# Kernel optimization log

Hardware: AMD Instinct MI355X
Metric: run time of the kernel (lower is better)

## Reference

```python
import jax, jax.numpy as jnp
import numpy as np

AGENT, WIN, DIM, HEADS = 6, 7, 256, 8


def _relative_position_index():
    # Exactly mirrors the torch buffer construction (meshgrid indexing='ij').
    coords = np.stack(np.meshgrid(np.arange(AGENT), np.arange(WIN), np.arange(WIN), indexing='ij'))
    cf = coords.reshape(3, -1)  # (3, N)
    rel = cf[:, :, None] - cf[:, None, :]  # (3, N, N)
    rel = np.transpose(rel, (1, 2, 0)).copy()  # (N, N, 3)
    rel[..., 0] += AGENT - 1
    rel[..., 1] += WIN - 1
    rel[..., 2] += WIN - 1
    rel[..., 0] *= (2 * WIN - 1) * (2 * WIN - 1)
    rel[..., 1] *= 2 * WIN - 1
    return rel.sum(-1).astype(np.int32)  # (N, N)


def setup_inputs() -> dict:
    key = jax.random.key(0)
    k1, k2, k3, k4 = jax.random.split(key, 4)
    b, X, Y = 1, 16, 16
    table_size = (2 * AGENT - 1) * (2 * WIN - 1) * (2 * WIN - 1)  # 1859
    x = jax.random.normal(k1, (b, AGENT, X, Y, WIN, WIN, DIM), dtype=jnp.float32)
    w_qkv = jax.random.normal(k2, (DIM, 3 * DIM), dtype=jnp.float32) * 0.02
    w_out = jax.random.normal(k3, (DIM, DIM), dtype=jnp.float32) * 0.02
    bias_table = jax.random.normal(k4, (table_size, HEADS), dtype=jnp.float32) * 0.02
    rel_index = jnp.asarray(_relative_position_index())
    return {"x": x, "w_qkv": w_qkv, "w_out": w_out, "bias_table": bias_table, "rel_index": rel_index}


def reference(x, w_qkv, w_out, bias_table, rel_index):
    b, L, X, Y, W1, W2, D = x.shape
    h = bias_table.shape[-1]
    dh = D // h
    scale = dh ** -0.5
    N = L * W1 * W2
    B = b * X * Y
    # 'b l x y w1 w2 d -> (b x y) (l w1 w2) d'
    xw = jnp.transpose(x, (0, 2, 3, 1, 4, 5, 6)).reshape(B, N, D)
    qkv = xw @ w_qkv  # (B, N, 3D)
    q, k, v = jnp.split(qkv, 3, axis=-1)
    def heads(t):
        return jnp.transpose(t.reshape(B, N, h, dh), (0, 2, 1, 3))  # (B, h, N, dh)
    q, k, v = heads(q) * scale, heads(k), heads(v)
    sim = jnp.einsum('bhid,bhjd->bhij', q, k)  # (B, h, N, N)
    bias = bias_table[rel_index]  # (N, N, h)
    sim = sim + jnp.transpose(bias, (2, 0, 1))[None]
    attn = jax.nn.softmax(sim, axis=-1)
    out = jnp.einsum('bhij,bhjd->bhid', attn, v)  # (B, h, N, dh)
    out = jnp.transpose(out, (0, 2, 1, 3)).reshape(B, N, h * dh)
    out = out @ w_out  # (B, N, D)
    out = out.reshape(b, X, Y, L, W1, W2, D)
    return jnp.transpose(out, (0, 3, 1, 2, 4, 5, 6))  # (b, l, x, y, w1, w2, d)
```

## Files before the change

kernel.cpp:

```cpp
#include <hip/hip_runtime.h>
#include <hip/hip_bf16.h>

#define NTOK 294
#define NB   256
#define NN   (NTOK*NTOK)
#define ROWS_M (NB*NTOK)
#define USN  19267584ULL

typedef __bf16 bf16x8 __attribute__((ext_vector_type(8)));
typedef float  f32x4  __attribute__((ext_vector_type(4)));
typedef unsigned short ushort_t;

union Bf8 { bf16x8 v; unsigned short u[8]; };

__device__ inline unsigned short f2bf(float f) {
    unsigned int u = __float_as_uint(f);
    return (unsigned short)((u + 0x7FFFu + ((u >> 16) & 1u)) >> 16);
}

__global__ void bias_expand(const float* __restrict__ table,
                            const int* __restrict__ rel,
                            float* __restrict__ biasQ) {
    int t = blockIdx.x * 256 + threadIdx.x;
    if (t >= NN) return;
    int idx = rel[t];
    const float* src = table + idx * 8;
#pragma unroll
    for (int h = 0; h < 8; ++h)
        biasQ[h * NN + t] = src[h];
}

__global__ __launch_bounds__(256) void qkv_gemm_mfma(const float* __restrict__ x,
                                                     const float* __restrict__ wqkv,
                                                     ushort_t* __restrict__ qb,
                                                     ushort_t* __restrict__ kb,
                                                     ushort_t* __restrict__ vt) {
    __shared__ unsigned short As[128 * 64];
    __shared__ unsigned short Bs[128 * 64];
    const int t    = threadIdx.x;
    const int lane = t & 63;
    const int w    = t >> 6;
    const int wm   = w >> 1, wn = w & 1;

    const int r  = t >> 1;
    const int h2 = t & 1;
    int m  = blockIdx.x * 128 + r;
    int Bi = m / NTOK, n = m - Bi * NTOK;
    int l  = n / 49,   ww = n - l * 49;
    int xx = Bi >> 4,  yy = Bi & 15;
    const float* arow = x + (size_t)((((l * 16 + xx) * 16 + yy) * 49 + ww) << 8) + h2 * 32;

    const int n4  = (t & 31) * 4;
    const int kl0 = (t >> 5) * 8;
    const int cb  = blockIdx.y * 128;
    const float* bsrc = wqkv + (size_t)kl0 * 768 + cb + n4;

    f32x4 acc[4][4];
#pragma unroll
    for (int i = 0; i < 4; ++i)
#pragma unroll
        for (int j = 0; j < 4; ++j) acc[i][j] = (f32x4){0.f, 0.f, 0.f, 0.f};

    for (int kk = 0; kk < 256; kk += 64) {
        Bf8 apk[4];
#pragma unroll
        for (int c = 0; c < 4; ++c) {
            float4 f0 = *(const float4*)(arow + kk + c * 8);
            float4 f1 = *(const float4*)(arow + kk + c * 8 + 4);
            apk[c].u[0] = f2bf(f0.x); apk[c].u[1] = f2bf(f0.y);
            apk[c].u[2] = f2bf(f0.z); apk[c].u[3] = f2bf(f0.w);
            apk[c].u[4] = f2bf(f1.x); apk[c].u[5] = f2bf(f1.y);
            apk[c].u[6] = f2bf(f1.z); apk[c].u[7] = f2bf(f1.w);
        }
        float bv[8][4];
#pragma unroll
        for (int e = 0; e < 8; ++e) {
            float4 f = *(const float4*)(bsrc + (size_t)(kk + e) * 768);
            bv[e][0] = f.x; bv[e][1] = f.y; bv[e][2] = f.z; bv[e][3] = f.w;
        }
        __syncthreads();
#pragma unroll
        for (int c = 0; c < 4; ++c) {
            int idx = (r * 64 + h2 * 32 + c * 8) ^ ((r & 7) << 3);
            *(bf16x8*)&As[idx] = apk[c].v;
        }
#pragma unroll
        for (int j = 0; j < 4; ++j) {
            Bf8 pk;
#pragma unroll
            for (int e = 0; e < 8; ++e) pk.u[e] = f2bf(bv[e][j]);
            int nn  = n4 + j;
            int idx = (nn * 64 + kl0) ^ ((nn & 7) << 3);
            *(bf16x8*)&Bs[idx] = pk.v;
        }
        __syncthreads();
        const int lrow = lane & 15;
        const int kofs = (lane >> 4) * 8;
#pragma unroll
        for (int ks = 0; ks < 2; ++ks) {
            bf16x8 af[4], bfr[4];
#pragma unroll
            for (int fi = 0; fi < 4; ++fi) {
                int rr  = wm * 64 + fi * 16 + lrow;
                int idx = (rr * 64 + ks * 32 + kofs) ^ ((rr & 7) << 3);
                af[fi] = *(const bf16x8*)&As[idx];
            }
#pragma unroll
            for (int fj = 0; fj < 4; ++fj) {
                int rr  = wn * 64 + fj * 16 + lrow;
                int idx = (rr * 64 + ks * 32 + kofs) ^ ((rr & 7) << 3);
                bfr[fj] = *(const bf16x8*)&Bs[idx];
            }
#pragma unroll
            for (int fi = 0; fi < 4; ++fi)
#pragma unroll
                for (int fj = 0; fj < 4; ++fj)
                    acc[fi][fj] = __builtin_amdgcn_mfma_f32_16x16x32_bf16(
                        af[fi], bfr[fj], acc[fi][fj], 0, 0, 0);
        }
    }

    const float scale = 0.17677669529663687f;
    const int rq   = lane >> 4;
    const int cidx = lane & 15;
#pragma unroll
    for (int fi = 0; fi < 4; ++fi) {
#pragma unroll
        for (int reg = 0; reg < 4; ++reg) {
            int mm  = blockIdx.x * 128 + wm * 64 + fi * 16 + rq * 4 + reg;
            int Bi2 = mm / NTOK, n2 = mm - Bi2 * NTOK;
#pragma unroll
            for (int fj = 0; fj < 4; ++fj) {
                int c     = cb + wn * 64 + fj * 16 + cidx;
                int which = c >> 8;
                int rr    = c & 255;
                int hh    = rr >> 5, di = rr & 31;
                int bhi   = Bi2 * 8 + hh;
                if (which == 0) {
                    qb[((size_t)bhi * NTOK + n2) * 32 + di] = f2bf(acc[fi][fj][reg] * scale);
                } else if (which == 1) {
                    kb[((size_t)bhi * NTOK + n2) * 32 + di] = f2bf(acc[fi][fj][reg]);
                } else {
                    vt[((size_t)bhi * 32 + di) * NTOK + n2] = f2bf(acc[fi][fj][reg]);
                }
            }
        }
    }
}

#define S_KS 40
#define S_VS 328
#define S_PS 40
__global__ __launch_bounds__(256) void attn_mfma(ushort_t* __restrict__ qb,
                                                 const ushort_t* __restrict__ kb,
                                                 const ushort_t* __restrict__ vt,
                                                 const float* __restrict__ biasQ) {
    __shared__ ushort_t ks[320 * S_KS];
    __shared__ ushort_t vs[32 * S_VS];
    __shared__ ushort_t ps[4 * 16 * S_PS];
    const int qt = blockIdx.x, bh = blockIdx.y, h = bh & 7;
    const int tid = threadIdx.x;

    const unsigned int* ksrc = (const unsigned int*)(kb + (size_t)bh * NTOK * 32);
    for (int t = tid; t < 294 * 16; t += 256) {
        int r = t >> 4, i = t & 15;
        *(unsigned int*)&ks[r * S_KS + 2 * i] = ksrc[t];
    }
    for (int t = tid; t < 26 * 16; t += 256) {
        int r = 294 + (t >> 4), i = t & 15;
        *(unsigned int*)&ks[r * S_KS + 2 * i] = 0u;
    }
    const unsigned int* vsrc = (const unsigned int*)(vt + (size_t)bh * 32 * NTOK);
    for (int t = tid; t < 32 * 147; t += 256) {
        int d = t / 147, i = t - d * 147;
        *(unsigned int*)&vs[d * S_VS + 2 * i] = vsrc[t];
    }
    for (int t = tid; t < 32 * 17; t += 256) {
        int d = t / 17, i = 147 + (t - d * 17);
        *(unsigned int*)&vs[d * S_VS + 2 * i] = 0u;
    }
    __syncthreads();

    const int wave = tid >> 6, lane = tid & 63;
    const int c = lane & 15, g = lane >> 4;
    const int q0 = qt * 128 + wave * 32;

    bf16x8 qf[2];
#pragma unroll
    for (int qs = 0; qs < 2; ++qs) {
        int qa = q0 + qs * 16 + c; if (qa > 293) qa = 293;
        qf[qs] = *(const bf16x8*)&qb[((size_t)bh * NTOK + qa) * 32 + 8 * g];
    }
    f32x4 acc_o[2][2];
    float psum[2][4];
#pragma unroll
    for (int qs = 0; qs < 2; ++qs) {
#pragma unroll
        for (int hf = 0; hf < 2; ++hf) acc_o[qs][hf] = (f32x4){0.f, 0.f, 0.f, 0.f};
#pragma unroll
        for (int rg = 0; rg < 4; ++rg) psum[qs][rg] = 0.f;
    }
    ushort_t* pw = ps + wave * 16 * S_PS;
    const float* bbase = biasQ + (size_t)h * NN;

    for (int kt = 0; kt < 10; ++kt) {
        const int kbase = kt * 32;
        bf16x8 kf[2], vf[2];
#pragma unroll
        for (int ksub = 0; ksub < 2; ++ksub)
            kf[ksub] = *(const bf16x8*)&ks[(kbase + ksub * 16 + c) * S_KS + 8 * g];
#pragma unroll
        for (int hf = 0; hf < 2; ++hf)
            vf[hf] = *(const bf16x8*)&vs[(hf * 16 + c) * S_VS + kbase + 8 * g];

#pragma unroll
        for (int qs = 0; qs < 2; ++qs) {
            f32x4 s0 = __builtin_amdgcn_mfma_f32_16x16x32_bf16(
                qf[qs], kf[0], (f32x4){0.f, 0.f, 0.f, 0.f}, 0, 0, 0);
            f32x4 s1 = __builtin_amdgcn_mfma_f32_16x16x32_bf16(
                qf[qs], kf[1], (f32x4){0.f, 0.f, 0.f, 0.f}, 0, 0, 0);
            const int qrb = q0 + qs * 16 + g * 4;
#pragma unroll
            for (int rg = 0; rg < 4; ++rg) {
                int qa = qrb + rg; if (qa > 293) qa = 293;
                const float* bp = bbase + (size_t)qa * NTOK;
#pragma unroll
                for (int ksub = 0; ksub < 2; ++ksub) {
                    int ka = kbase + ksub * 16 + c;
                    int kc = ka > 293 ? 293 : ka;
                    float bias = (ka < NTOK) ? bp[kc] : -1e4f;
                    float s = (ksub ? s1[rg] : s0[rg]) + bias;
                    float p = __expf(s);
                    psum[qs][rg] += p;
                    pw[(g * 4 + rg) * S_PS + ksub * 16 + c] = f2bf(p);
                }
            }
            bf16x8 pa = *(const bf16x8*)&pw[c * S_PS + 8 * g];
#pragma unroll
            for (int hf = 0; hf < 2; ++hf)
                acc_o[qs][hf] = __builtin_amdgcn_mfma_f32_16x16x32_bf16(
                    pa, vf[hf], acc_o[qs][hf], 0, 0, 0);
        }
    }

#pragma unroll
    for (int qs = 0; qs < 2; ++qs)
#pragma unroll
        for (int rg = 0; rg < 4; ++rg) {
            float v = psum[qs][rg];
            v += __shfl_xor(v, 1); v += __shfl_xor(v, 2);
            v += __shfl_xor(v, 4); v += __shfl_xor(v, 8);
            psum[qs][rg] = 1.0f / v;
        }

#pragma unroll
    for (int qs = 0; qs < 2; ++qs) {
        const int qrb = q0 + qs * 16 + g * 4;
#pragma unroll
        for (int rg = 0; rg < 4; ++rg) {
            int qa = qrb + rg;
            if (qa < NTOK) {
#pragma unroll
                for (int hf = 0; hf < 2; ++hf) {
                    float val = acc_o[qs][hf][rg] * psum[qs][rg];
                    qb[((size_t)bh * NTOK + qa) * 32 + hf * 16 + c] = f2bf(val);
                }
            }
        }
    }
}

__global__ __launch_bounds__(256) void out_gemm_mfma(const ushort_t* __restrict__ ob,
                                                     const float* __restrict__ wout,
                                                     float* __restrict__ out) {
    __shared__ unsigned short As[128 * 64];
    __shared__ unsigned short Bs[128 * 64];
    const int t    = threadIdx.x;
    const int lane = t & 63;
    const int w    = t >> 6;
    const int wm   = w >> 1, wn = w & 1;

    const int r  = t >> 1;
    const int h2 = t & 1;
    int m  = blockIdx.x * 128 + r;
    int Bi = m / NTOK, n = m - Bi * NTOK;

    const int n4  = (t & 31) * 4;
    const int kl0 = (t >> 5) * 8;
    const int cb  = blockIdx.y * 128;
    const float* bsrc = wout + (size_t)kl0 * 256 + cb + n4;

    f32x4 acc[4][4];
#pragma unroll
    for (int i = 0; i < 4; ++i)
#pragma unroll
        for (int j = 0; j < 4; ++j) acc[i][j] = (f32x4){0.f, 0.f, 0.f, 0.f};

    for (int kk = 0; kk < 256; kk += 64) {
        const int h_idx = (kk >> 5) + h2;
        const ushort_t* asrc = ob + ((size_t)(Bi * 8 + h_idx) * NTOK + n) * 32;
        bf16x8 apk[4];
#pragma unroll
        for (int c = 0; c < 4; ++c) apk[c] = *(const bf16x8*)&asrc[c * 8];
        float bv[8][4];
#pragma unroll
        for (int e = 0; e < 8; ++e) {
            float4 f = *(const float4*)(bsrc + (size_t)(kk + e) * 256);
            bv[e][0] = f.x; bv[e][1] = f.y; bv[e][2] = f.z; bv[e][3] = f.w;
        }
        __syncthreads();
#pragma unroll
        for (int c = 0; c < 4; ++c) {
            int idx = (r * 64 + h2 * 32 + c * 8) ^ ((r & 7) << 3);
            *(bf16x8*)&As[idx] = apk[c];
        }
#pragma unroll
        for (int j = 0; j < 4; ++j) {
            Bf8 pk;
#pragma unroll
            for (int e = 0; e < 8; ++e) pk.u[e] = f2bf(bv[e][j]);
            int nn  = n4 + j;
            int idx = (nn * 64 + kl0) ^ ((nn & 7) << 3);
            *(bf16x8*)&Bs[idx] = pk.v;
        }
        __syncthreads();
        const int lrow = lane & 15;
        const int kofs = (lane >> 4) * 8;
#pragma unroll
        for (int ks = 0; ks < 2; ++ks) {
            bf16x8 af[4], bfr[4];
#pragma unroll
            for (int fi = 0; fi < 4; ++fi) {
                int rr  = wm * 64 + fi * 16 + lrow;
                int idx = (rr * 64 + ks * 32 + kofs) ^ ((rr & 7) << 3);
                af[fi] = *(const bf16x8*)&As[idx];
            }
#pragma unroll
            for (int fj = 0; fj < 4; ++fj) {
                int rr  = wn * 64 + fj * 16 + lrow;
                int idx = (rr * 64 + ks * 32 + kofs) ^ ((rr & 7) << 3);
                bfr[fj] = *(const bf16x8*)&Bs[idx];
            }
#pragma unroll
            for (int fi = 0; fi < 4; ++fi)
#pragma unroll
                for (int fj = 0; fj < 4; ++fj)
                    acc[fi][fj] = __builtin_amdgcn_mfma_f32_16x16x32_bf16(
                        af[fi], bfr[fj], acc[fi][fj], 0, 0, 0);
        }
    }

    const int rq   = lane >> 4;
    const int cidx = lane & 15;
#pragma unroll
    for (int fi = 0; fi < 4; ++fi) {
#pragma unroll
        for (int reg = 0; reg < 4; ++reg) {
            int mm  = blockIdx.x * 128 + wm * 64 + fi * 16 + rq * 4 + reg;
            int Bi2 = mm / NTOK, n2 = mm - Bi2 * NTOK;
            int l2  = n2 / 49,   w2 = n2 - l2 * 49;
            int xx2 = Bi2 >> 4,  yy2 = Bi2 & 15;
            float* orow = out + (size_t)((((l2 * 16 + xx2) * 16 + yy2) * 49 + w2) << 8);
#pragma unroll
            for (int fj = 0; fj < 4; ++fj) {
                int c = cb + wn * 64 + fj * 16 + cidx;
                orow[c] = acc[fi][fj][reg];
            }
        }
    }
}

extern "C" void kernel_launch(void* const* d_in, const int* in_sizes, int n_in,
                              void* d_out, int out_size, void* d_ws, size_t ws_size,
                              hipStream_t stream) {
    const float* x     = (const float*)d_in[0];
    const float* wqkv  = (const float*)d_in[1];
    const float* wout  = (const float*)d_in[2];
    const float* table = (const float*)d_in[3];
    const int*   rel   = (const int*)d_in[4];
    float* out = (float*)d_out;

    ushort_t* qb    = (ushort_t*)d_ws;
    ushort_t* kb    = qb + USN;
    ushort_t* vt    = kb + USN;
    float*    biasQ = (float*)(vt + USN);

    hipLaunchKernelGGL(bias_expand, dim3((NN + 255) / 256), dim3(256), 0, stream,
                       table, rel, biasQ);
    hipLaunchKernelGGL(qkv_gemm_mfma, dim3(ROWS_M / 128, 6), dim3(256), 0, stream,
                       x, wqkv, qb, kb, vt);
    hipLaunchKernelGGL(attn_mfma, dim3(3, 2048), dim3(256), 0, stream,
                       qb, kb, vt, biasQ);
    hipLaunchKernelGGL(out_gemm_mfma, dim3(ROWS_M / 128, 2), dim3(256), 0, stream,
                       qb, wout, out);
}
```

Baseline: 430.4 us.

## Pre-transpose weights to bf16 and load MFMA fragments directly from global memory

Adds a prep kernel that converts and transposes w_qkv and w_out to bf16 once per call. The QKV and output GEMMs drop their shared-memory staging and barriers, and each lane loads its MFMA fragments straight from global memory. The grid is reordered so the column tiles of the same row block run adjacently and can share the cached A rows. This removes the LDS round-trip, the per-block weight conversion and the syncthreads, in exchange for redundant global/L2 traffic across waves and an extra small kernel launch.

```diff
diff --git a/kernel.cpp b/kernel.cpp
--- a/kernel.cpp
+++ b/kernel.cpp
@@ -16,6 +16,13 @@
 __device__ inline unsigned short f2bf(float f) {
     unsigned int u = __float_as_uint(f);
     return (unsigned short)((u + 0x7FFFu + ((u >> 16) & 1u)) >> 16);
+}
+
+__device__ inline bf16x8 cvt8(float4 a, float4 b) {
+    bf16x8 r;
+    r[0] = (__bf16)a.x; r[1] = (__bf16)a.y; r[2] = (__bf16)a.z; r[3] = (__bf16)a.w;
+    r[4] = (__bf16)b.x; r[5] = (__bf16)b.y; r[6] = (__bf16)b.z; r[7] = (__bf16)b.w;
+    return r;
 }
 
 __global__ void bias_expand(const float* __restrict__ table,
@@ -30,30 +37,49 @@
         biasQ[h * NN + t] = src[h];
 }
 
-__global__ __launch_bounds__(256) void qkv_gemm_mfma(const float* __restrict__ x,
-                                                     const float* __restrict__ wqkv,
-                                                     ushort_t* __restrict__ qb,
-                                                     ushort_t* __restrict__ kb,
-                                                     ushort_t* __restrict__ vt) {
-    __shared__ unsigned short As[128 * 64];
-    __shared__ unsigned short Bs[128 * 64];
+__global__ void wt_prep(const float* __restrict__ wqkv,
+                        const float* __restrict__ wout,
+                        ushort_t* __restrict__ wqkvT,
+                        ushort_t* __restrict__ woutT) {
+    int t = blockIdx.x * 256 + threadIdx.x;
+    if (t < 768 * 256) {
+        int n = t >> 8, k = t & 255;
+        wqkvT[t] = f2bf(wqkv[k * 768 + n]);
+    } else {
+        int u = t - 768 * 256;
+        int n = u >> 8, k = u & 255;
+        woutT[u] = f2bf(wout[k * 256 + n]);
+    }
+}
+
+__global__ __launch_bounds__(256) void qkv_gemm_mfma2(const float* __restrict__ x,
+                                                      const ushort_t* __restrict__ wqkvT,
+                                                      ushort_t* __restrict__ qb,
+                                                      ushort_t* __restrict__ kb,
+                                                      ushort_t* __restrict__ vt) {
     const int t    = threadIdx.x;
     const int lane = t & 63;
     const int w    = t >> 6;
     const int wm   = w >> 1, wn = w & 1;
-
-    const int r  = t >> 1;
-    const int h2 = t & 1;
-    int m  = blockIdx.x * 128 + r;
-    int Bi = m / NTOK, n = m - Bi * NTOK;
-    int l  = n / 49,   ww = n - l * 49;
-    int xx = Bi >> 4,  yy = Bi & 15;
-    const float* arow = x + (size_t)((((l * 16 + xx) * 16 + yy) * 49 + ww) << 8) + h2 * 32;
-
-    const int n4  = (t & 31) * 4;
-    const int kl0 = (t >> 5) * 8;
-    const int cb  = blockIdx.y * 128;
-    const float* bsrc = wqkv + (size_t)kl0 * 768 + cb + n4;
+    const int l15  = lane & 15, kg8 = (lane >> 4) * 8;
+    const int cb   = blockIdx.x * 128;
+    const int mt   = blockIdx.y * 128;
+
+    const float* arow[4];
+#pragma unroll
+    for (int fi = 0; fi < 4; ++fi) {
+        int m  = mt + wm * 64 + fi * 16 + l15;
+        int Bi = m / NTOK, n = m - Bi * NTOK;
+        int l  = n / 49,   ww = n - l * 49;
+        int xx = Bi >> 4,  yy = Bi & 15;
+        arow[fi] = x + (size_t)((((l * 16 + xx) * 16 + yy) * 49 + ww) << 8) + kg8;
+    }
+    const ushort_t* brow[4];
+#pragma unroll
+    for (int fj = 0; fj < 4; ++fj) {
+        int nn = cb + wn * 64 + fj * 16 + l15;
+        brow[fj] = wqkvT + (size_t)nn * 256 + kg8;
+    }
 
     f32x4 acc[4][4];
 #pragma unroll
@@ -61,63 +87,24 @@
 #pragma unroll
         for (int j = 0; j < 4; ++j) acc[i][j] = (f32x4){0.f, 0.f, 0.f, 0.f};
 
-    for (int kk = 0; kk < 256; kk += 64) {
-        Bf8 apk[4];
-#pragma unroll
-        for (int c = 0; c < 4; ++c) {
-            float4 f0 = *(const float4*)(arow + kk + c * 8);
-            float4 f1 = *(const float4*)(arow + kk + c * 8 + 4);
-            apk[c].u[0] = f2bf(f0.x); apk[c].u[1] = f2bf(f0.y);
-            apk[c].u[2] = f2bf(f0.z); apk[c].u[3] = f2bf(f0.w);
-            apk[c].u[4] = f2bf(f1.x); apk[c].u[5] = f2bf(f1.y);
-            apk[c].u[6] = f2bf(f1.z); apk[c].u[7] = f2bf(f1.w);
-        }
-        float bv[8][4];
-#pragma unroll
-        for (int e = 0; e < 8; ++e) {
-            float4 f = *(const float4*)(bsrc + (size_t)(kk + e) * 768);
-            bv[e][0] = f.x; bv[e][1] = f.y; bv[e][2] = f.z; bv[e][3] = f.w;
-        }
-        __syncthreads();
-#pragma unroll
-        for (int c = 0; c < 4; ++c) {
-            int idx = (r * 64 + h2 * 32 + c * 8) ^ ((r & 7) << 3);
-            *(bf16x8*)&As[idx] = apk[c].v;
-        }
-#pragma unroll
-        for (int j = 0; j < 4; ++j) {
-            Bf8 pk;
-#pragma unroll
-            for (int e = 0; e < 8; ++e) pk.u[e] = f2bf(bv[e][j]);
-            int nn  = n4 + j;
-            int idx = (nn * 64 + kl0) ^ ((nn & 7) << 3);
-            *(bf16x8*)&Bs[idx] = pk.v;
-        }
-        __syncthreads();
-        const int lrow = lane & 15;
-        const int kofs = (lane >> 4) * 8;
-#pragma unroll
-        for (int ks = 0; ks < 2; ++ks) {
-            bf16x8 af[4], bfr[4];
-#pragma unroll
-            for (int fi = 0; fi < 4; ++fi) {
-                int rr  = wm * 64 + fi * 16 + lrow;
-                int idx = (rr * 64 + ks * 32 + kofs) ^ ((rr & 7) << 3);
-                af[fi] = *(const bf16x8*)&As[idx];
-            }
-#pragma unroll
-            for (int fj = 0; fj < 4; ++fj) {
-                int rr  = wn * 64 + fj * 16 + lrow;
-                int idx = (rr * 64 + ks * 32 + kofs) ^ ((rr & 7) << 3);
-                bfr[fj] = *(const bf16x8*)&Bs[idx];
-            }
-#pragma unroll
-            for (int fi = 0; fi < 4; ++fi)
-#pragma unroll
-                for (int fj = 0; fj < 4; ++fj)
-                    acc[fi][fj] = __builtin_amdgcn_mfma_f32_16x16x32_bf16(
-                        af[fi], bfr[fj], acc[fi][fj], 0, 0, 0);
-        }
+#pragma unroll 2
+    for (int kk = 0; kk < 256; kk += 32) {
+        bf16x8 af[4], bfr[4];
+#pragma unroll
+        for (int fi = 0; fi < 4; ++fi) {
+            float4 f0 = *(const float4*)(arow[fi] + kk);
+            float4 f1 = *(const float4*)(arow[fi] + kk + 4);
+            af[fi] = cvt8(f0, f1);
+        }
+#pragma unroll
+        for (int fj = 0; fj < 4; ++fj)
+            bfr[fj] = *(const bf16x8*)(brow[fj] + kk);
+#pragma unroll
+        for (int fi = 0; fi < 4; ++fi)
+#pragma unroll
+            for (int fj = 0; fj < 4; ++fj)
+                acc[fi][fj] = __builtin_amdgcn_mfma_f32_16x16x32_bf16(
+                    af[fi], bfr[fj], acc[fi][fj], 0, 0, 0);
     }
 
     const float scale = 0.17677669529663687f;
@@ -127,7 +114,7 @@
     for (int fi = 0; fi < 4; ++fi) {
 #pragma unroll
         for (int reg = 0; reg < 4; ++reg) {
-            int mm  = blockIdx.x * 128 + wm * 64 + fi * 16 + rq * 4 + reg;
+            int mm  = mt + wm * 64 + fi * 16 + rq * 4 + reg;
             int Bi2 = mm / NTOK, n2 = mm - Bi2 * NTOK;
 #pragma unroll
             for (int fj = 0; fj < 4; ++fj) {
@@ -270,25 +257,30 @@
     }
 }
 
-__global__ __launch_bounds__(256) void out_gemm_mfma(const ushort_t* __restrict__ ob,
-                                                     const float* __restrict__ wout,
-                                                     float* __restrict__ out) {
-    __shared__ unsigned short As[128 * 64];
-    __shared__ unsigned short Bs[128 * 64];
+__global__ __launch_bounds__(256) void out_gemm_mfma2(const ushort_t* __restrict__ ob,
+                                                      const ushort_t* __restrict__ woutT,
+                                                      float* __restrict__ out) {
     const int t    = threadIdx.x;
     const int lane = t & 63;
     const int w    = t >> 6;
     const int wm   = w >> 1, wn = w & 1;
-
-    const int r  = t >> 1;
-    const int h2 = t & 1;
-    int m  = blockIdx.x * 128 + r;
-    int Bi = m / NTOK, n = m - Bi * NTOK;
-
-    const int n4  = (t & 31) * 4;
-    const int kl0 = (t >> 5) * 8;
-    const int cb  = blockIdx.y * 128;
-    const float* bsrc = wout + (size_t)kl0 * 256 + cb + n4;
+    const int l15  = lane & 15, kg8 = (lane >> 4) * 8;
+    const int cb   = blockIdx.x * 128;
+    const int mt   = blockIdx.y * 128;
+
+    const ushort_t* abase[4];
+#pragma unroll
+    for (int fi = 0; fi < 4; ++fi) {
+        int m  = mt + wm * 64 + fi * 16 + l15;
+        int Bi = m / NTOK, n = m - Bi * NTOK;
+        abase[fi] = ob + ((size_t)(Bi * 8) * NTOK + n) * 32 + kg8;
+    }
+    const ushort_t* brow[4];
+#pragma unroll
+    for (int fj = 0; fj < 4; ++fj) {
+        int nn = cb + wn * 64 + fj * 16 + l15;
+        brow[fj] = woutT + (size_t)nn * 256 + kg8;
+    }
 
     f32x4 acc[4][4];
 #pragma unroll
@@ -296,58 +288,22 @@
 #pragma unroll
         for (int j = 0; j < 4; ++j) acc[i][j] = (f32x4){0.f, 0.f, 0.f, 0.f};
 
-    for (int kk = 0; kk < 256; kk += 64) {
-        const int h_idx = (kk >> 5) + h2;
-        const ushort_t* asrc = ob + ((size_t)(Bi * 8 + h_idx) * NTOK + n) * 32;
-        bf16x8 apk[4];
-#pragma unroll
-        for (int c = 0; c < 4; ++c) apk[c] = *(const bf16x8*)&asrc[c * 8];
-        float bv[8][4];
-#pragma unroll
-        for (int e = 0; e < 8; ++e) {
-            float4 f = *(const float4*)(bsrc + (size_t)(kk + e) * 256);
-            bv[e][0] = f.x; bv[e][1] = f.y; bv[e][2] = f.z; bv[e][3] = f.w;
-        }
-        __syncthreads();
-#pragma unroll
-        for (int c = 0; c < 4; ++c) {
-            int idx = (r * 64 + h2 * 32 + c * 8) ^ ((r & 7) << 3);
-            *(bf16x8*)&As[idx] = apk[c];
-        }
-#pragma unroll
-        for (int j = 0; j < 4; ++j) {
-            Bf8 pk;
-#pragma unroll
-            for (int e = 0; e < 8; ++e) pk.u[e] = f2bf(bv[e][j]);
-            int nn  = n4 + j;
-            int idx = (nn * 64 + kl0) ^ ((nn & 7) << 3);
-            *(bf16x8*)&Bs[idx] = pk.v;
-        }
-        __syncthreads();
-        const int lrow = lane & 15;
-        const int kofs = (lane >> 4) * 8;
-#pragma unroll
-        for (int ks = 0; ks < 2; ++ks) {
-            bf16x8 af[4], bfr[4];
-#pragma unroll
-            for (int fi = 0; fi < 4; ++fi) {
-                int rr  = wm * 64 + fi * 16 + lrow;
-                int idx = (rr * 64 + ks * 32 + kofs) ^ ((rr & 7) << 3);
-                af[fi] = *(const bf16x8*)&As[idx];
-            }
-#pragma unroll
-            for (int fj = 0; fj < 4; ++fj) {
-                int rr  = wn * 64 + fj * 16 + lrow;
-                int idx = (rr * 64 + ks * 32 + kofs) ^ ((rr & 7) << 3);
-                bfr[fj] = *(const bf16x8*)&Bs[idx];
-            }
-#pragma unroll
-            for (int fi = 0; fi < 4; ++fi)
-#pragma unroll
-                for (int fj = 0; fj < 4; ++fj)
-                    acc[fi][fj] = __builtin_amdgcn_mfma_f32_16x16x32_bf16(
-                        af[fi], bfr[fj], acc[fi][fj], 0, 0, 0);
-        }
+#pragma unroll 2
+    for (int kk = 0; kk < 256; kk += 32) {
+        const int hstep = kk >> 5;
+        bf16x8 af[4], bfr[4];
+#pragma unroll
+        for (int fi = 0; fi < 4; ++fi)
+            af[fi] = *(const bf16x8*)(abase[fi] + (size_t)hstep * NTOK * 32);
+#pragma unroll
+        for (int fj = 0; fj < 4; ++fj)
+            bfr[fj] = *(const bf16x8*)(brow[fj] + kk);
+#pragma unroll
+        for (int fi = 0; fi < 4; ++fi)
+#pragma unroll
+            for (int fj = 0; fj < 4; ++fj)
+                acc[fi][fj] = __builtin_amdgcn_mfma_f32_16x16x32_bf16(
+                    af[fi], bfr[fj], acc[fi][fj], 0, 0, 0);
     }
 
     const int rq   = lane >> 4;
@@ -356,7 +312,7 @@
     for (int fi = 0; fi < 4; ++fi) {
 #pragma unroll
         for (int reg = 0; reg < 4; ++reg) {
-            int mm  = blockIdx.x * 128 + wm * 64 + fi * 16 + rq * 4 + reg;
+            int mm  = mt + wm * 64 + fi * 16 + rq * 4 + reg;
             int Bi2 = mm / NTOK, n2 = mm - Bi2 * NTOK;
             int l2  = n2 / 49,   w2 = n2 - l2 * 49;
             int xx2 = Bi2 >> 4,  yy2 = Bi2 & 15;
@@ -384,13 +340,17 @@
     ushort_t* kb    = qb + USN;
     ushort_t* vt    = kb + USN;
     float*    biasQ = (float*)(vt + USN);
+    ushort_t* wqkvT = (ushort_t*)(biasQ + 8 * NN);
+    ushort_t* woutT = wqkvT + 768 * 256;
 
     hipLaunchKernelGGL(bias_expand, dim3((NN + 255) / 256), dim3(256), 0, stream,
                        table, rel, biasQ);
-    hipLaunchKernelGGL(qkv_gemm_mfma, dim3(ROWS_M / 128, 6), dim3(256), 0, stream,
-                       x, wqkv, qb, kb, vt);
+    hipLaunchKernelGGL(wt_prep, dim3((768 * 256 + 256 * 256) / 256), dim3(256), 0, stream,
+                       wqkv, wout, wqkvT, woutT);
+    hipLaunchKernelGGL(qkv_gemm_mfma2, dim3(6, 588), dim3(256), 0, stream,
+                       x, wqkvT, qb, kb, vt);
     hipLaunchKernelGGL(attn_mfma, dim3(3, 2048), dim3(256), 0, stream,
                        qb, kb, vt, biasQ);
-    hipLaunchKernelGGL(out_gemm_mfma, dim3(ROWS_M / 128, 2), dim3(256), 0, stream,
-                       qb, wout, out);
-}
+    hipLaunchKernelGGL(out_gemm_mfma2, dim3(2, 588), dim3(256), 0, stream,
+                       qb, woutT, out);
+}
```

Measured after the change: 489.2 us. 13.7% more time.
